# Optimization experiments

Hardware: AMD Instinct MI355X
Metric: run time of the kernel (lower is better)

## Reference

```python
import jax, jax.numpy as jnp
import numpy as np

N_EMBD = 2560
N_HEAD = 32
HEAD_DIM = N_EMBD // N_HEAD  # 80
ROTARY_DIM = 32
SEQ = 2048
BSZ = 1


def _rope_tables(seq_len, rotary_dim, base=10000.0):
    inv_freq = 1.0 / (base ** (np.arange(0, rotary_dim, 2, dtype=np.float32) / rotary_dim))
    t = np.arange(seq_len, dtype=np.float32)
    freqs = np.outer(t, inv_freq)                      # [S, rd/2]
    emb = np.concatenate([freqs, freqs], axis=-1)      # [S, rd]
    return jnp.asarray(np.cos(emb)), jnp.asarray(np.sin(emb))


def setup_inputs() -> dict:
    key = jax.random.key(0)
    k1, k2, k3, k4, k5 = jax.random.split(key, 5)
    op_size = HEAD_DIM * (N_HEAD + 2 * N_HEAD)  # fused q,k,v => 3*n_embd
    hidden_states = jax.random.normal(k1, (BSZ, SEQ, N_EMBD), dtype=jnp.float32)
    Wqkv_w = jax.random.normal(k2, (op_size, N_EMBD), dtype=jnp.float32) * 0.02
    Wqkv_b = jax.random.normal(k3, (op_size,), dtype=jnp.float32) * 0.02
    out_w = jax.random.normal(k4, (N_EMBD, N_EMBD), dtype=jnp.float32) * 0.02
    out_b = jax.random.normal(k5, (N_EMBD,), dtype=jnp.float32) * 0.02
    cos, sin = _rope_tables(SEQ, ROTARY_DIM)
    return {"hidden_states": hidden_states, "Wqkv_w": Wqkv_w, "Wqkv_b": Wqkv_b,
            "out_w": out_w, "out_b": out_b, "cos": cos, "sin": sin}


def apply_partial_rotary(x, cos, sin):
    # x: [S, B, H, D]; cos/sin: [S, rd]
    rd = cos.shape[-1]
    c = cos[:, None, None, :]
    s = sin[:, None, None, :]
    x_rot = x[..., :rd]
    # NOTE: faithful to source -- rotated half is concatenated WITHOUT negation
    tmp = jnp.concatenate([x[..., rd // 2:rd], x[..., :rd // 2]], axis=-1)
    rotten = x_rot * c + tmp * s
    return jnp.concatenate([rotten, x[..., rd:]], axis=-1)


def reference(hidden_states, Wqkv_w, Wqkv_b, out_w, out_b, cos, sin):
    bsz, q_len, _ = hidden_states.shape
    qkv = hidden_states @ Wqkv_w.T + Wqkv_b            # [B, S, 3*E]
    q, k, v = jnp.split(qkv, 3, axis=-1)
    # [B, S, H, D] -> [S, B, H, D] for rotary
    q = q.reshape(bsz, q_len, N_HEAD, HEAD_DIM).transpose(1, 0, 2, 3)
    k = k.reshape(bsz, q_len, N_HEAD, HEAD_DIM).transpose(1, 0, 2, 3)
    v = v.reshape(bsz, q_len, N_HEAD, HEAD_DIM).transpose(0, 2, 1, 3)  # [B, H, S, D]
    cos_t, sin_t = cos[:q_len], sin[:q_len]
    q = apply_partial_rotary(q, cos_t, sin_t).transpose(1, 2, 0, 3)    # [B, H, S, D]
    k = apply_partial_rotary(k, cos_t, sin_t).transpose(1, 2, 0, 3)    # [B, H, S, D]
    scale = 1.0 / jnp.sqrt(jnp.asarray(HEAD_DIM, dtype=q.dtype))
    scores = jnp.einsum('bhqd,bhkd->bhqk', q, k) * scale
    causal = jnp.tril(jnp.ones((q_len, q_len), dtype=bool))
    scores = jnp.where(causal, scores, jnp.asarray(-1e30, dtype=scores.dtype))
    probs = jax.nn.softmax(scores, axis=-1)
    out = jnp.einsum('bhqk,bhkd->bhqd', probs, v)       # [B, H, S, D]
    out = out.transpose(0, 2, 1, 3).reshape(bsz, q_len, N_EMBD)
    return out @ out_w.T + out_b
```

## Files before the change

### kernel.cpp

```cpp
#include <hip/hip_runtime.h>
#include <cstdint>
#include <cstddef>

typedef unsigned short bf16_t;
typedef __attribute__((ext_vector_type(8))) short bf16x8;
typedef __attribute__((ext_vector_type(4))) float f32x4;

__device__ __forceinline__ float bf2f(bf16_t b) {
  unsigned int u = ((unsigned int)b) << 16;
  return __builtin_bit_cast(float, u);
}
__device__ __forceinline__ bf16_t f2bf(float f) {
  unsigned int u = __builtin_bit_cast(unsigned int, f);
  u += 0x7fffu + ((u >> 16) & 1u);
  return (bf16_t)(u >> 16);
}

constexpr int SEQ = 2048, NE = 2560, NH = 32, HD = 80, OP = 7680;

__global__ void cvt3(const float* __restrict__ s0, const float* __restrict__ s1,
                     const float* __restrict__ s2, bf16_t* __restrict__ d0,
                     bf16_t* __restrict__ d1, bf16_t* __restrict__ d2)
{
  constexpr int N0 = SEQ * NE / 4, N1 = OP * NE / 4;
  int t = blockIdx.x * 256 + threadIdx.x;
  const float* s; bf16_t* d;
  if (t < N0)            { s = s0; d = d0; }
  else if (t < N0 + N1)  { s = s1; d = d1; t -= N0; }
  else                   { s = s2; d = d2; t -= N0 + N1; }
  float4 v = ((const float4*)s)[t];
  ushort4 o;
  o.x = f2bf(v.x); o.y = f2bf(v.y); o.z = f2bf(v.z); o.w = f2bf(v.w);
  ((ushort4*)d)[t] = o;
}

__device__ __forceinline__ void store_out(bf16_t* p, float v) { *p = f2bf(v); }
__device__ __forceinline__ void store_out(float* p, float v)  { *p = v; }

template <typename OutT>
__global__ __launch_bounds__(256, 2) void gemm_bt_bias(
    const bf16_t* __restrict__ A,
    const bf16_t* __restrict__ B,
    const float*  __restrict__ bias,
    OutT* __restrict__ C,
    int M, int N, int K)
{
  __shared__ bf16_t As[128 * 32];
  __shared__ bf16_t Bs[128 * 32];

  const int tid  = threadIdx.x;
  const int lane = tid & 63;
  const int wave = tid >> 6;
  const int m0 = blockIdx.y * 128;
  const int n0 = blockIdx.x * 128;
  const int mw = (wave >> 1) * 64;
  const int nw = (wave & 1) * 64;
  const int lm = lane & 15;
  const int lq = lane >> 4;

  f32x4 acc[4][4];
#pragma unroll
  for (int i = 0; i < 4; ++i)
#pragma unroll
    for (int j = 0; j < 4; ++j)
      acc[i][j] = (f32x4){0.f, 0.f, 0.f, 0.f};

  const int ldr = lane >> 2;
  const int ldc = (lane & 3) * 8;

  for (int kt = 0; kt < K; kt += 32) {
#pragma unroll
    for (int r = 0; r < 2; ++r) {
      const int seg = wave * 2 + r;
      const int row = seg * 16 + ldr;
      const bf16_t* ga = A + (size_t)(m0 + row) * K + kt + ldc;
      const bf16_t* gb = B + (size_t)(n0 + row) * K + kt + ldc;
      __builtin_amdgcn_global_load_lds(
          (const __attribute__((address_space(1))) unsigned int*)ga,
          (__attribute__((address_space(3))) unsigned int*)&As[seg * 512], 16, 0, 0);
      __builtin_amdgcn_global_load_lds(
          (const __attribute__((address_space(1))) unsigned int*)gb,
          (__attribute__((address_space(3))) unsigned int*)&Bs[seg * 512], 16, 0, 0);
    }
    __syncthreads();

    bf16x8 af[4], bfq[4];
#pragma unroll
    for (int i = 0; i < 4; ++i)
      af[i] = *(const bf16x8*)&As[(mw + i * 16 + lm) * 32 + lq * 8];
#pragma unroll
    for (int j = 0; j < 4; ++j)
      bfq[j] = *(const bf16x8*)&Bs[(nw + j * 16 + lm) * 32 + lq * 8];

#pragma unroll
    for (int i = 0; i < 4; ++i)
#pragma unroll
      for (int j = 0; j < 4; ++j)
        acc[i][j] = __builtin_amdgcn_mfma_f32_16x16x32_bf16(af[i], bfq[j], acc[i][j], 0, 0, 0);

    __syncthreads();
  }

#pragma unroll
  for (int i = 0; i < 4; ++i) {
#pragma unroll
    for (int j = 0; j < 4; ++j) {
      const int n = n0 + nw + j * 16 + lm;
      const float bv = bias[n];
#pragma unroll
      for (int r = 0; r < 4; ++r) {
        const int m = m0 + mw + i * 16 + lq * 4 + r;
        store_out(&C[(size_t)m * N + n], acc[i][j][r] + bv);
      }
    }
  }
}

__global__ void rope_kernel(bf16_t* __restrict__ qkv,
                            const float* __restrict__ cosb,
                            const float* __restrict__ sinb)
{
  const int t = blockIdx.x * 256 + threadIdx.x;
  const int i  = t & 15;
  const int qk = (t >> 4) & 1;
  const int h  = (t >> 5) & 31;
  const int s  = t >> 10;
  const size_t base = (size_t)s * OP + qk * NE + h * HD;
  const float xi = bf2f(qkv[base + i]);
  const float xj = bf2f(qkv[base + i + 16]);
  const float c1 = cosb[s * 32 + i];
  const float s1 = sinb[s * 32 + i];
  const float c2 = cosb[s * 32 + i + 16];
  const float s2 = sinb[s * 32 + i + 16];
  qkv[base + i]      = f2bf(xi * c1 + xj * s1);
  qkv[base + i + 16] = f2bf(xj * c2 + xi * s2);
}

constexpr int KSTR = 96;
constexpr int VSTR = 72;
constexpr int PSTR = 72;

__global__ __launch_bounds__(256, 4) void attn_mfma(
    const bf16_t* __restrict__ qkv, bf16_t* __restrict__ aout)
{
  __shared__ bf16_t Ks[64 * KSTR];
  __shared__ bf16_t Vt[80 * VSTR];
  __shared__ bf16_t Ps[4][16 * PSTR];

  const int h    = blockIdx.y;
  const int qt   = (int)gridDim.x - 1 - blockIdx.x;
  const int q0   = qt * 64;
  const int tid  = threadIdx.x;
  const int lane = tid & 63;
  const int wave = tid >> 6;
  const int lm   = lane & 15;
  const int quad = lane >> 4;

  const int qg = q0 + 16 * wave + lm;

  const int koff = NE + h * HD;
  const int voff = 2 * NE + h * HD;
  const float SC = 0.1118033988749895f;

  bf16x8 qf[3];
  {
    const bf16_t* q_r = qkv + (size_t)qg * OP + h * HD;
#pragma unroll
    for (int ks = 0; ks < 3; ++ks) {
      const int col = ks * 32 + quad * 8;
      if (col < 80) qf[ks] = *(const bf16x8*)(q_r + col);
      else          qf[ks] = (bf16x8){0,0,0,0,0,0,0,0};
    }
  }

  int kofs[3];
#pragma unroll
  for (int r = 0; r < 3; ++r) {
    const int e = (wave * 3 + r) * 512 + lane * 8;
    const int row = e / 96, c = e % 96;
    kofs[r] = row * OP + (c < 80 ? c : c - 16);
  }

  const int vp = tid & 31;
  const int vg = tid >> 5;

  f32x4 oacc[5];
#pragma unroll
  for (int mt = 0; mt < 5; ++mt) oacc[mt] = (f32x4){0.f,0.f,0.f,0.f};
  float lsum = 0.f;

  const int ntiles = qt + 1;
  for (int t = 0; t < ntiles; ++t) {
    const int kb = t * 64;

#pragma unroll
    for (int r = 0; r < 3; ++r) {
      const bf16_t* g = qkv + (size_t)kb * OP + koff + kofs[r];
      __builtin_amdgcn_global_load_lds(
          (const __attribute__((address_space(1))) unsigned int*)g,
          (__attribute__((address_space(3))) unsigned int*)&Ks[(wave * 3 + r) * 512],
          16, 0, 0);
    }
    {
      const bf16_t* va = qkv + (size_t)(kb + 2 * vp) * OP + voff + vg * 10;
      const bf16_t* vb = va + OP;
      unsigned int wa[5], wb[5];
#pragma unroll
      for (int j = 0; j < 5; ++j) {
        wa[j] = *(const unsigned int*)(va + 2 * j);
        wb[j] = *(const unsigned int*)(vb + 2 * j);
      }
#pragma unroll
      for (int tt = 0; tt < 10; ++tt) {
        const unsigned int A = wa[tt >> 1], B = wb[tt >> 1];
        const unsigned int pk = (tt & 1) ? ((A >> 16) | (B & 0xffff0000u))
                                         : ((A & 0xffffu) | (B << 16));
        *(unsigned int*)&Vt[(vg * 10 + tt) * VSTR + 2 * vp] = pk;
      }
    }
    __syncthreads();

    f32x4 sacc[4];
#pragma unroll
    for (int mt = 0; mt < 4; ++mt) sacc[mt] = (f32x4){0.f,0.f,0.f,0.f};
#pragma unroll
    for (int ks = 0; ks < 3; ++ks) {
      bf16x8 kf[4];
#pragma unroll
      for (int mt = 0; mt < 4; ++mt)
        kf[mt] = *(const bf16x8*)&Ks[(mt * 16 + lm) * KSTR + ks * 32 + quad * 8];
#pragma unroll
      for (int mt = 0; mt < 4; ++mt)
        sacc[mt] = __builtin_amdgcn_mfma_f32_16x16x32_bf16(kf[mt], qf[ks], sacc[mt], 0, 0, 0);
    }

    const int keyb = kb + quad * 4;
#pragma unroll
    for (int mt = 0; mt < 4; ++mt) {
      float ps[4];
#pragma unroll
      for (int r = 0; r < 4; ++r) {
        float p = __expf(sacc[mt][r] * SC);
        p = (keyb + mt * 16 + r > qg) ? 0.f : p;
        ps[r] = p;
      }
      lsum += (ps[0] + ps[1]) + (ps[2] + ps[3]);
      ushort4 pk;
      pk.x = f2bf(ps[0]); pk.y = f2bf(ps[1]); pk.z = f2bf(ps[2]); pk.w = f2bf(ps[3]);
      *(ushort4*)&Ps[wave][lm * PSTR + mt * 16 + quad * 4] = pk;
    }

#pragma unroll
    for (int ks = 0; ks < 2; ++ks) {
      bf16x8 vf[5], pf;
#pragma unroll
      for (int mt = 0; mt < 5; ++mt)
        vf[mt] = *(const bf16x8*)&Vt[(mt * 16 + lm) * VSTR + ks * 32 + quad * 8];
      pf = *(const bf16x8*)&Ps[wave][lm * PSTR + ks * 32 + quad * 8];
#pragma unroll
      for (int mt = 0; mt < 5; ++mt)
        oacc[mt] = __builtin_amdgcn_mfma_f32_16x16x32_bf16(vf[mt], pf, oacc[mt], 0, 0, 0);
    }
    __syncthreads();
  }

  lsum += __shfl_xor(lsum, 16);
  lsum += __shfl_xor(lsum, 32);
  const float inv = 1.f / lsum;
  bf16_t* base = aout + (size_t)qg * NE + h * HD + quad * 4;
#pragma unroll
  for (int mt = 0; mt < 5; ++mt) {
    ushort4 st;
    st.x = f2bf(oacc[mt][0] * inv);
    st.y = f2bf(oacc[mt][1] * inv);
    st.z = f2bf(oacc[mt][2] * inv);
    st.w = f2bf(oacc[mt][3] * inv);
    *(ushort4*)(base + mt * 16) = st;
  }
}

extern "C" void kernel_launch(void* const* d_in, const int* in_sizes, int n_in,
                              void* d_out, int out_size, void* d_ws, size_t ws_size,
                              hipStream_t stream)
{
  const float* hs   = (const float*)d_in[0];
  const float* wqkv = (const float*)d_in[1];
  const float* bqkv = (const float*)d_in[2];
  const float* wout = (const float*)d_in[3];
  const float* bout = (const float*)d_in[4];
  const float* cosb = (const float*)d_in[5];
  const float* sinb = (const float*)d_in[6];

  bf16_t* hs_bf   = (bf16_t*)d_ws;
  bf16_t* wqkv_bf = hs_bf   + (size_t)SEQ * NE;
  bf16_t* wout_bf = wqkv_bf + (size_t)OP * NE;
  bf16_t* qkv     = wout_bf + (size_t)NE * NE;
  bf16_t* aout    = qkv     + (size_t)SEQ * OP;
  float*  out     = (float*)d_out;

  constexpr int CVT_T = (SEQ * NE + OP * NE + NE * NE) / 4;
  cvt3<<<CVT_T / 256, 256, 0, stream>>>(hs, wqkv, wout, hs_bf, wqkv_bf, wout_bf);

  gemm_bt_bias<bf16_t><<<dim3(OP / 128, SEQ / 128), 256, 0, stream>>>(
      hs_bf, wqkv_bf, bqkv, qkv, SEQ, OP, NE);
  rope_kernel<<<(SEQ * NH * 2 * 16) / 256, 256, 0, stream>>>(qkv, cosb, sinb);
  attn_mfma<<<dim3(SEQ / 64, NH), 256, 0, stream>>>(qkv, aout);
  gemm_bt_bias<float><<<dim3(NE / 128, SEQ / 128), 256, 0, stream>>>(
      aout, wout_bf, bout, out, SEQ, NE, NE);
}
```

Measured before the change: 434.5 us.

## Split-K the output projection and double the GEMM K-step per barrier

The GEMM now stages two 32-wide K sub-tiles in LDS per iteration, so each barrier pair covers a 64-wide K step instead of 32. The output-projection GEMM is split along K into two halves via blockIdx.z, which doubles the block count to fill more CUs. The fp32 partial results go to workspace, reusing the bf16 input and weight buffers that are dead after the QKV GEMM. A new reduce kernel adds the two partials plus the bias. The cost is extra global traffic for writing and reading the partials, plus one more kernel launch.

Measured after the change: 432.1 us. About the same (-0.6%).

```diff
diff --git a/kernel.cpp b/kernel.cpp
--- a/kernel.cpp
+++ b/kernel.cpp
@@ -43,16 +43,18 @@
     const bf16_t* __restrict__ B,
     const float*  __restrict__ bias,
     OutT* __restrict__ C,
-    int M, int N, int K)
-{
-  __shared__ bf16_t As[128 * 32];
-  __shared__ bf16_t Bs[128 * 32];
+    int M, int N, int K, int klen)
+{
+  __shared__ bf16_t As[2][128 * 32];
+  __shared__ bf16_t Bs[2][128 * 32];
 
   const int tid  = threadIdx.x;
   const int lane = tid & 63;
   const int wave = tid >> 6;
   const int m0 = blockIdx.y * 128;
   const int n0 = blockIdx.x * 128;
+  const int kbeg = blockIdx.z * klen;
+  OutT* Cz = C + (size_t)blockIdx.z * M * N;
   const int mw = (wave >> 1) * 64;
   const int nw = (wave & 1) * 64;
   const int lm = lane & 15;
@@ -68,35 +70,42 @@
   const int ldr = lane >> 2;
   const int ldc = (lane & 3) * 8;
 
-  for (int kt = 0; kt < K; kt += 32) {
-#pragma unroll
-    for (int r = 0; r < 2; ++r) {
-      const int seg = wave * 2 + r;
-      const int row = seg * 16 + ldr;
-      const bf16_t* ga = A + (size_t)(m0 + row) * K + kt + ldc;
-      const bf16_t* gb = B + (size_t)(n0 + row) * K + kt + ldc;
-      __builtin_amdgcn_global_load_lds(
-          (const __attribute__((address_space(1))) unsigned int*)ga,
-          (__attribute__((address_space(3))) unsigned int*)&As[seg * 512], 16, 0, 0);
-      __builtin_amdgcn_global_load_lds(
-          (const __attribute__((address_space(1))) unsigned int*)gb,
-          (__attribute__((address_space(3))) unsigned int*)&Bs[seg * 512], 16, 0, 0);
+  for (int kt = kbeg; kt < kbeg + klen; kt += 64) {
+#pragma unroll
+    for (int sub = 0; sub < 2; ++sub) {
+#pragma unroll
+      for (int r = 0; r < 2; ++r) {
+        const int seg = wave * 2 + r;
+        const int row = seg * 16 + ldr;
+        const int col = kt + sub * 32 + ldc;
+        const bf16_t* ga = A + (size_t)(m0 + row) * K + col;
+        const bf16_t* gb = B + (size_t)(n0 + row) * K + col;
+        __builtin_amdgcn_global_load_lds(
+            (const __attribute__((address_space(1))) unsigned int*)ga,
+            (__attribute__((address_space(3))) unsigned int*)&As[sub][seg * 512], 16, 0, 0);
+        __builtin_amdgcn_global_load_lds(
+            (const __attribute__((address_space(1))) unsigned int*)gb,
+            (__attribute__((address_space(3))) unsigned int*)&Bs[sub][seg * 512], 16, 0, 0);
+      }
     }
     __syncthreads();
 
-    bf16x8 af[4], bfq[4];
-#pragma unroll
-    for (int i = 0; i < 4; ++i)
-      af[i] = *(const bf16x8*)&As[(mw + i * 16 + lm) * 32 + lq * 8];
-#pragma unroll
-    for (int j = 0; j < 4; ++j)
-      bfq[j] = *(const bf16x8*)&Bs[(nw + j * 16 + lm) * 32 + lq * 8];
-
-#pragma unroll
-    for (int i = 0; i < 4; ++i)
+#pragma unroll
+    for (int sub = 0; sub < 2; ++sub) {
+      bf16x8 af[4], bfq[4];
+#pragma unroll
+      for (int i = 0; i < 4; ++i)
+        af[i] = *(const bf16x8*)&As[sub][(mw + i * 16 + lm) * 32 + lq * 8];
 #pragma unroll
       for (int j = 0; j < 4; ++j)
-        acc[i][j] = __builtin_amdgcn_mfma_f32_16x16x32_bf16(af[i], bfq[j], acc[i][j], 0, 0, 0);
+        bfq[j] = *(const bf16x8*)&Bs[sub][(nw + j * 16 + lm) * 32 + lq * 8];
+
+#pragma unroll
+      for (int i = 0; i < 4; ++i)
+#pragma unroll
+        for (int j = 0; j < 4; ++j)
+          acc[i][j] = __builtin_amdgcn_mfma_f32_16x16x32_bf16(af[i], bfq[j], acc[i][j], 0, 0, 0);
+    }
 
     __syncthreads();
   }
@@ -106,14 +115,27 @@
 #pragma unroll
     for (int j = 0; j < 4; ++j) {
       const int n = n0 + nw + j * 16 + lm;
-      const float bv = bias[n];
+      const float bv = bias ? bias[n] : 0.f;
 #pragma unroll
       for (int r = 0; r < 4; ++r) {
         const int m = m0 + mw + i * 16 + lq * 4 + r;
-        store_out(&C[(size_t)m * N + n], acc[i][j][r] + bv);
-      }
-    }
-  }
+        store_out(&Cz[(size_t)m * N + n], acc[i][j][r] + bv);
+      }
+    }
+  }
+}
+
+__global__ void reduce2_bias(const float* __restrict__ p, const float* __restrict__ bias,
+                             float* __restrict__ out)
+{
+  const int t = blockIdx.x * 256 + threadIdx.x;
+  const float4 a = ((const float4*)p)[t];
+  const float4 b = ((const float4*)(p + (size_t)SEQ * NE))[t];
+  const float4 bv = ((const float4*)bias)[t % (NE / 4)];
+  float4 r;
+  r.x = a.x + b.x + bv.x; r.y = a.y + b.y + bv.y;
+  r.z = a.z + b.z + bv.z; r.w = a.w + b.w + bv.w;
+  ((float4*)out)[t] = r;
 }
 
 __global__ void rope_kernel(bf16_t* __restrict__ qkv,
@@ -297,14 +319,16 @@
   bf16_t* qkv     = wout_bf + (size_t)NE * NE;
   bf16_t* aout    = qkv     + (size_t)SEQ * OP;
   float*  out     = (float*)d_out;
+  float*  pbuf    = (float*)d_ws;
 
   constexpr int CVT_T = (SEQ * NE + OP * NE + NE * NE) / 4;
   cvt3<<<CVT_T / 256, 256, 0, stream>>>(hs, wqkv, wout, hs_bf, wqkv_bf, wout_bf);
 
-  gemm_bt_bias<bf16_t><<<dim3(OP / 128, SEQ / 128), 256, 0, stream>>>(
-      hs_bf, wqkv_bf, bqkv, qkv, SEQ, OP, NE);
+  gemm_bt_bias<bf16_t><<<dim3(OP / 128, SEQ / 128, 1), 256, 0, stream>>>(
+      hs_bf, wqkv_bf, bqkv, qkv, SEQ, OP, NE, NE);
   rope_kernel<<<(SEQ * NH * 2 * 16) / 256, 256, 0, stream>>>(qkv, cosb, sinb);
   attn_mfma<<<dim3(SEQ / 64, NH), 256, 0, stream>>>(qkv, aout);
-  gemm_bt_bias<float><<<dim3(NE / 128, SEQ / 128), 256, 0, stream>>>(
-      aout, wout_bf, bout, out, SEQ, NE, NE);
-}
+  gemm_bt_bias<float><<<dim3(NE / 128, SEQ / 128, 2), 256, 0, stream>>>(
+      aout, wout_bf, nullptr, pbuf, SEQ, NE, NE, NE / 2);
+  reduce2_bias<<<(SEQ * NE / 4) / 256, 256, 0, stream>>>(pbuf, bout, out);
+}
```
